# Kernel tuning notes

Measured on AMD Instinct MI355X. Metric: run time of the kernel, lower is better.

## Reference

```python
import jax, jax.numpy as jnp
import numpy as np

B, S, D = 2, 2048, 1024
H = 16            # attention heads
KVH = 4           # key/value heads
G = H // KVH      # group_size = 4
HD = D // H       # head_dim = 64
ROPE_THETA = 10000.0


def rope(x):
    # x: [B, S, D]; interleaved-pair rotary embedding over full last dim
    d = x.shape[-1]
    inv_freq = 1.0 / (ROPE_THETA ** (jnp.arange(0, d, 2, dtype=jnp.float32) / d))  # [d/2]
    ang = jnp.arange(x.shape[1], dtype=jnp.float32)[:, None] * inv_freq[None, :]   # [S, d/2]
    cos, sin = jnp.cos(ang), jnp.sin(ang)
    x1, x2 = x[..., 0::2], x[..., 1::2]
    r1 = x1 * cos - x2 * sin
    r2 = x1 * sin + x2 * cos
    out = jnp.stack([r1, r2], axis=-1).reshape(x.shape)
    return out


def setup_inputs() -> dict:
    key = jax.random.key(0)
    kx, kq, kk, kv = jax.random.split(key, 4)
    x = jax.random.normal(kx, (B, S, D), dtype=jnp.float32)
    # mark last 256 positions of batch element 1 as padding via NaN
    x = x.at[1, S - 256:, :].set(jnp.nan)
    scale = 1.0 / np.sqrt(D)
    Wq = jax.random.normal(kq, (D, D), dtype=jnp.float32) * scale
    Wk = jax.random.normal(kk, (D, D // G), dtype=jnp.float32) * scale
    Wv = jax.random.normal(kv, (D, D // G), dtype=jnp.float32) * scale
    return {"x": x, "Wq": Wq, "Wk": Wk, "Wv": Wv}


def reference(x, Wq, Wk, Wv):
    pad = jnp.isnan(x)                      # [B,S,D]
    x = jnp.where(pad, 0.0, x)
    key_pad = jnp.any(pad, axis=-1)         # [B,S] True = padded token

    q = x @ Wq                              # [B,S,D]
    k = jnp.repeat(x @ Wk, G, axis=-1)      # grouped KV, repeat_interleave -> [B,S,D]
    v = jnp.repeat(x @ Wv, G, axis=-1)

    q = rope(q)
    k = rope(k)

    def split_heads(t):
        return t.reshape(B, S, H, HD).transpose(0, 2, 1, 3)  # [B,H,S,HD]

    q, k, v = split_heads(q), split_heads(k), split_heads(v)

    scores = jnp.einsum('bhqd,bhkd->bhqk', q, k) / np.sqrt(HD)
    causal = jnp.tril(jnp.ones((S, S), dtype=bool))
    allow = causal[None, None, :, :] & (~key_pad)[:, None, None, :]
    scores = jnp.where(allow, scores, -1e9)
    attn = jax.nn.softmax(scores, axis=-1)
    out = jnp.einsum('bhqk,bhkd->bhqd', attn, v)
    return out.transpose(0, 2, 1, 3).reshape(B, S, D)
```

## Files before the change

kernel.cpp:

```cpp
#include <hip/hip_runtime.h>
#include <hip/hip_bf16.h>
#include <math.h>

typedef unsigned short u16;
typedef unsigned int u32;
typedef __bf16 bf16x8 __attribute__((ext_vector_type(8)));
typedef float fx4 __attribute__((ext_vector_type(4)));

#define MFMA16(a, b, c) __builtin_amdgcn_mfma_f32_16x16x32_bf16(a, b, c, 0, 0, 0)

static constexpr int Bb = 2, Ss = 2048, Dd = 1024, Hh = 16, DKV = 256;
static constexpr int NQKV = 1536;
static constexpr int ROWS = Bb * Ss;
static constexpr float L2T_OVER = 0.0259525632f;
static constexpr float SC2 = 0.18033688f;
static constexpr int PSTR = 76;

__device__ __forceinline__ u16 f2bf(float f) {
    union { float f; u32 i; } v; v.f = f;
    u32 u = v.i;
    return (u16)((u + 0x7FFFu + ((u >> 16) & 1u)) >> 16);
}
__device__ __forceinline__ u16 bfr(float f) {
    return (u16)((__float_as_uint(f) + 0x8000u) >> 16);
}

__device__ __forceinline__ void gl16(const u16* g, u16* l) {
    __builtin_amdgcn_global_load_lds(
        (const __attribute__((address_space(1))) void*)g,
        (__attribute__((address_space(3))) void*)l, 16, 0, 0);
}

template <int CTRL>
__device__ __forceinline__ float dppf(float x) {
    return __int_as_float(
        __builtin_amdgcn_mov_dpp(__float_as_int(x), CTRL, 0xF, 0xF, true));
}
__device__ __forceinline__ float rsum16(float x) {
    x += dppf<0xB1>(x);
    x += dppf<0x4E>(x);
    x += dppf<0x124>(x);
    x += dppf<0x128>(x);
    return x;
}

__global__ void pre_kernel(const float* __restrict__ x, const float* __restrict__ Wq,
                           const float* __restrict__ Wk, const float* __restrict__ Wv,
                           u16* __restrict__ xc, u32* __restrict__ kpb,
                           u16* __restrict__ wAll) {
    __shared__ u16 tile[32][33];
    __shared__ int flag;
    int bid = blockIdx.x, t = threadIdx.x;
    if (bid < 4096) {
        int row = bid;
        if (t == 0) flag = 0;
        __syncthreads();
        float4 d = *(const float4*)(x + (size_t)row * Dd + t * 4);
        int any = 0;
        float a0 = d.x, a1 = d.y, a2 = d.z, a3 = d.w;
        if ((__float_as_uint(a0) & 0x7FFFFFFFu) > 0x7F800000u) { a0 = 0.f; any = 1; }
        if ((__float_as_uint(a1) & 0x7FFFFFFFu) > 0x7F800000u) { a1 = 0.f; any = 1; }
        if ((__float_as_uint(a2) & 0x7FFFFFFFu) > 0x7F800000u) { a2 = 0.f; any = 1; }
        if ((__float_as_uint(a3) & 0x7FFFFFFFu) > 0x7F800000u) { a3 = 0.f; any = 1; }
        if (any) atomicOr(&flag, 1);
        uint2 o;
        o.x = (u32)f2bf(a0) | ((u32)f2bf(a1) << 16);
        o.y = (u32)f2bf(a2) | ((u32)f2bf(a3) << 16);
        *(uint2*)(xc + (size_t)row * Dd + t * 4) = o;
        __syncthreads();
        if (t == 0 && flag) {
            int b = row >> 11, s = row & (Ss - 1);
            atomicOr(&kpb[b * 64 + (s >> 5)], 1u << (s & 31));
        }
        return;
    }
    const float* in; u16* out; int C, bx, by;
    if (bid < 5120) { int i = bid - 4096; in = Wq; out = wAll; C = Dd; bx = i & 31; by = i >> 5; }
    else if (bid < 5376) { int i = bid - 5120; in = Wk; out = wAll + (size_t)Dd * Dd; C = DKV; bx = i & 7; by = i >> 3; }
    else { int i = bid - 5376; in = Wv; out = wAll + (size_t)1280 * Dd; C = DKV; bx = i & 7; by = i >> 3; }
    int c0 = bx * 32, r0 = by * 32;
    int tx = t & 31, ty = t >> 5;
    for (int i = 0; i < 32; i += 8)
        tile[ty + i][tx] = f2bf(in[(size_t)(r0 + ty + i) * C + c0 + tx]);
    __syncthreads();
    for (int i = 0; i < 32; i += 8)
        out[(size_t)(c0 + ty + i) * Dd + r0 + tx] = tile[tx][ty + i];
}

__global__ __launch_bounds__(256) void gemm_qkv(
    const u16* __restrict__ A, const u16* __restrict__ Bt, u16* __restrict__ C) {
    __shared__ __align__(16) u16 As[2][128 * 32];
    __shared__ __align__(16) u16 Bs[2][64 * 32];
    int t = threadIdx.x, w = t >> 6, lane = t & 63;
    int l15 = lane & 15, quad = lane >> 4;
    int col0 = blockIdx.x * 64, row0 = blockIdx.y * 128;
    int wm = w >> 1, wn = w & 1;
    fx4 acc[4][2];
#pragma unroll
    for (int i = 0; i < 4; ++i)
#pragma unroll
        for (int j = 0; j < 2; ++j) acc[i][j] = (fx4){0.f, 0.f, 0.f, 0.f};

    auto stage = [&](int kb, int buf) {
#pragma unroll
        for (int i = 0; i < 2; ++i) {
            int slot = i * 256 + t;
            int row = slot >> 2, p = slot & 3, g = p ^ ((row >> 1) & 3);
            gl16(A + (size_t)(row0 + row) * Dd + kb * 32 + g * 8,
                 &As[buf][(i * 256 + w * 64) * 8]);
        }
        {
            int row = t >> 2, p = t & 3, g = p ^ ((row >> 1) & 3);
            gl16(Bt + (size_t)(col0 + row) * Dd + kb * 32 + g * 8,
                 &Bs[buf][(w * 64) * 8]);
        }
    };

    stage(0, 0);
    int buf = 0;
    for (int kb = 0; kb < 32; ++kb) {
        __syncthreads();
        if (kb + 1 < 32) stage(kb + 1, buf ^ 1);
        bf16x8 af[4], bfr2[2];
#pragma unroll
        for (int mi = 0; mi < 4; ++mi) {
            int row = wm * 64 + mi * 16 + l15;
            af[mi] = *(const bf16x8*)(&As[buf][row * 32 + ((quad ^ ((row >> 1) & 3)) * 8)]);
        }
#pragma unroll
        for (int ni = 0; ni < 2; ++ni) {
            int row = wn * 32 + ni * 16 + l15;
            bfr2[ni] = *(const bf16x8*)(&Bs[buf][row * 32 + ((quad ^ ((row >> 1) & 3)) * 8)]);
        }
#pragma unroll
        for (int mi = 0; mi < 4; ++mi)
#pragma unroll
            for (int ni = 0; ni < 2; ++ni)
                acc[mi][ni] = MFMA16(af[mi], bfr2[ni], acc[mi][ni]);
        buf ^= 1;
    }
#pragma unroll
    for (int mi = 0; mi < 4; ++mi) {
        int rbase = row0 + wm * 64 + mi * 16 + quad * 4;
#pragma unroll
        for (int ni = 0; ni < 2; ++ni) {
            int ccol = col0 + wn * 32 + ni * 16 + l15;
#pragma unroll
            for (int r = 0; r < 4; ++r)
                C[(size_t)(rbase + r) * NQKV + ccol] = f2bf(acc[mi][ni][r]);
        }
    }
}

__global__ void post_kernel(const u16* __restrict__ qkv, u16* __restrict__ kr,
                            u16* __restrict__ vtb) {
    __shared__ u16 tile[32][33];
    int bid = blockIdx.x, t = threadIdx.x;
    if (bid < 4096) {
        int row = bid;
        float pos = (float)(row & (Ss - 1));
        float kv = __uint_as_float(((u32)qkv[(size_t)row * NQKV + Dd + t]) << 16);
        float j0 = (float)(2 * t), j1 = j0 + 1.0f;
        float f0 = exp2f(-j0 * L2T_OVER), f1 = exp2f(-j1 * L2T_OVER);
        float s0, c0, s1, c1;
        sincosf(pos * f0, &s0, &c0);
        sincosf(pos * f1, &s1, &c1);
        float r0 = kv * (c0 - s0), r1 = kv * (s0 + c0);
        float r2 = kv * (c1 - s1), r3 = kv * (s1 + c1);
        uint2 o;
        o.x = (u32)f2bf(r0) | ((u32)f2bf(r1) << 16);
        o.y = (u32)f2bf(r2) | ((u32)f2bf(r3) << 16);
        *(uint2*)(kr + (size_t)row * Dd + t * 4) = o;
        return;
    }
    int i = bid - 4096;
    int b = i >> 9, by = (i & 511) >> 3, bx = i & 7;
    int c0 = bx * 32, r0 = by * 32;
    int tx = t & 31, ty = t >> 5;
    for (int k = 0; k < 32; k += 8)
        tile[ty + k][tx] = qkv[(size_t)(b * Ss + r0 + ty + k) * NQKV + 1280 + c0 + tx];
    __syncthreads();
    for (int k = 0; k < 32; k += 8)
        vtb[(size_t)(b * DKV + c0 + ty + k) * Ss + r0 + tx] = tile[tx][ty + k];
}

__device__ __forceinline__ bf16x8 ropeFrag(uint4 raw, float pos, float jbase) {
    u32 W[4] = {raw.x, raw.y, raw.z, raw.w};
    union { u32 u[4]; bf16x8 v; } o;
#pragma unroll
    for (int c = 0; c < 4; ++c) {
        float x0 = __uint_as_float(W[c] << 16);
        float x1 = __uint_as_float(W[c] & 0xFFFF0000u);
        float f = exp2f(-(jbase + (float)c) * L2T_OVER);
        float sn, cs;
        sincosf(pos * f, &sn, &cs);
        float r0 = x0 * cs - x1 * sn, r1 = x0 * sn + x1 * cs;
        o.u[c] = (u32)f2bf(r0) | ((u32)f2bf(r1) << 16);
    }
    return o.v;
}

__global__ __launch_bounds__(256) void attn_kernel(
    const u16* __restrict__ qkv, const u16* __restrict__ kr,
    const u16* __restrict__ vt, const u32* __restrict__ kpb,
    float* __restrict__ out) {
    __shared__ __align__(16) u16 Ks[2][64 * 64];
    __shared__ __align__(16) u16 Vs[2][16 * 64];
    __shared__ __align__(16) u16 Ps[4][16 * PSTR];

    int t = threadIdx.x, w = t >> 6, lane = t & 63;
    int l15 = lane & 15, quad = lane >> 4;
    int bid = blockIdx.x;
    int u = bid >> 5, g = u >> 3, i = u & 7;
    int tile = (g == 0) ? (31 - i) : (g == 1) ? (16 + i) : (g == 2) ? (15 - i) : i;
    int hh = bid & 31, b = hh >> 4, h = hh & 15;
    int q0 = tile * 64;
    int nkb = tile + 1;

    int pos = q0 + w * 16 + l15;
    const u16* qp = qkv + (size_t)(b * Ss + pos) * NQKV + h * 64;
    float jb = (float)(h * 32 + quad * 4);
    bf16x8 qf0 = ropeFrag(*(const uint4*)(qp + quad * 8), (float)pos, jb);
    bf16x8 qf1 = ropeFrag(*(const uint4*)(qp + 32 + quad * 8), (float)pos, jb + 16.f);

    u32 pw_all = kpb[b * 64 + lane];

    auto stageK = [&](int k0, int buf) {
#pragma unroll
        for (int i2 = 0; i2 < 2; ++i2) {
            int row = i2 * 32 + w * 8 + (lane >> 3);
            int gg = (lane & 7) ^ (row & 7);
            gl16(kr + (size_t)(b * Ss + k0 + row) * Dd + h * 64 + gg * 8,
                 &Ks[buf][(i2 * 32 + w * 8) * 64]);
        }
    };
    auto stageV = [&](int k0, int buf) {
        if (w < 2) {
            int row = w * 8 + (lane >> 3);
            int gg = (lane & 7) ^ (row & 7);
            gl16(vt + (size_t)(b * DKV + h * 16 + row) * Ss + k0 + gg * 8,
                 &Vs[buf][(w * 8) * 64]);
        }
    };

    float l_lane[4] = {0.f, 0.f, 0.f, 0.f};
    fx4 oacc = (fx4){0.f, 0.f, 0.f, 0.f};

    stageK(0, 0);
    stageV(0, 0);
    int buf = 0;
    const int qrb = q0 + w * 16 + quad * 4;
    const int qmin = q0 + w * 16;

    for (int kb = 0; kb < nkb; ++kb) {
        int k0 = kb * 64;
        __syncthreads();
        if (kb + 1 < nkb) { stageK(k0 + 64, buf ^ 1); stageV(k0 + 64, buf ^ 1); }

        fx4 s[4];
#pragma unroll
        for (int tt = 0; tt < 4; ++tt) {
            const u16* kb_ = &Ks[buf][(tt * 16 + l15) * 64];
            bf16x8 kf0 = *(const bf16x8*)(kb_ + ((quad ^ (l15 & 7)) * 8));
            bf16x8 kf1 = *(const bf16x8*)(kb_ + (((quad + 4) ^ (l15 & 7)) * 8));
            fx4 z = (fx4){0.f, 0.f, 0.f, 0.f};
            fx4 a = MFMA16(qf0, kf0, z);
            s[tt] = MFMA16(qf1, kf1, a);
        }

        u32 pw0 = (u32)__shfl((int)pw_all, 2 * kb, 64);
        u32 pw1 = (u32)__shfl((int)pw_all, 2 * kb + 1, 64);
        bool fast = (k0 + 63 <= qmin) & ((pw0 | pw1) == 0u);

        float e[4][4];
        if (fast) {
#pragma unroll
            for (int tt = 0; tt < 4; ++tt)
#pragma unroll
                for (int r = 0; r < 4; ++r)
                    e[tt][r] = exp2f(fmaf(s[tt][r], SC2, -32.f));
        } else {
            u32 padb[4];
#pragma unroll
            for (int tt = 0; tt < 4; ++tt)
                padb[tt] = ((tt & 2 ? pw1 : pw0) >> ((tt * 16 + l15) & 31)) & 1u;
#pragma unroll
            for (int r = 0; r < 4; ++r) {
                int qq = qrb + r;
#pragma unroll
                for (int tt = 0; tt < 4; ++tt) {
                    float ee = exp2f(fmaf(s[tt][r], SC2, -32.f));
                    e[tt][r] = (k0 + tt * 16 + l15 <= qq && !padb[tt]) ? ee : 0.f;
                }
            }
        }

#pragma unroll
        for (int r = 0; r < 4; ++r) {
            l_lane[r] += (e[0][r] + e[1][r]) + (e[2][r] + e[3][r]);
            int prow = (quad * 4 + r) * PSTR + l15;
            Ps[w][prow + 0] = bfr(e[0][r]);
            Ps[w][prow + 16] = bfr(e[1][r]);
            Ps[w][prow + 32] = bfr(e[2][r]);
            Ps[w][prow + 48] = bfr(e[3][r]);
        }

#pragma unroll
        for (int hh2 = 0; hh2 < 2; ++hh2) {
            bf16x8 vf = *(const bf16x8*)(&Vs[buf][l15 * 64 + (((quad + 4 * hh2) ^ (l15 & 7)) * 8)]);
            bf16x8 pf = *(const bf16x8*)(&Ps[w][l15 * PSTR + hh2 * 32 + quad * 8]);
            oacc = MFMA16(pf, vf, oacc);
        }
        buf ^= 1;
    }

#pragma unroll
    for (int r = 0; r < 4; ++r) {
        float l_row = rsum16(l_lane[r]);
        float a = oacc[r] / l_row;
        float4 o4 = {a, a, a, a};
        *(float4*)(out + (size_t)(b * Ss + qrb + r) * Dd + h * 64 + l15 * 4) = o4;
    }
}

extern "C" void kernel_launch(void* const* d_in, const int* in_sizes, int n_in,
                              void* d_out, int out_size, void* d_ws, size_t ws_size,
                              hipStream_t stream) {
    const float* x = (const float*)d_in[0];
    const float* Wq = (const float*)d_in[1];
    const float* Wk = (const float*)d_in[2];
    const float* Wv = (const float*)d_in[3];
    float* out = (float*)d_out;

    char* ws = (char*)d_ws;
    const size_t SZ_XC = (size_t)ROWS * Dd * 2;
    const size_t SZ_KPB = 4096;
    const size_t SZ_WALL = (size_t)NQKV * Dd * 2;
    const size_t SZ_QKV = (size_t)ROWS * NQKV * 2;

    size_t off = 0;
    u16* xc = (u16*)(ws + off);
    u16* krope = (u16*)(ws + off); off += SZ_XC;
    u32* kpb = (u32*)(ws + off); off += SZ_KPB;
    u16* wAll = (u16*)(ws + off);
    u16* vtb = (u16*)(ws + off); off += SZ_WALL;
    u16* qkv = (u16*)(ws + off); off += SZ_QKV;
    (void)ws_size; (void)in_sizes; (void)n_in; (void)out_size;

    hipMemsetAsync(kpb, 0, 2 * 64 * 4, stream);
    pre_kernel<<<5632, 256, 0, stream>>>(x, Wq, Wk, Wv, xc, kpb, wAll);
    gemm_qkv<<<dim3(NQKV / 64, ROWS / 128), 256, 0, stream>>>(xc, wAll, qkv);
    post_kernel<<<5120, 256, 0, stream>>>(qkv, krope, vtb);
    attn_kernel<<<1024, 256, 0, stream>>>(qkv, krope, vtb, kpb, out);
}
```

Measured before the change: 152.9 us.

## Pair causal query tiles per block to share K/V staging and balance work

Each attention block now handles two query tiles, p and 31-p. Every block therefore walks the same total number of key blocks, and the K/V tiles it stages in LDS are reused for both query tiles. The grid is halved from 1024 to 512 blocks and the P scratch buffer is doubled. This removes the causal load imbalance and redundant K/V loads for the short tiles. The cost is fewer blocks in flight on a 256-CU part and more registers per thread.

```diff
diff --git a/kernel.cpp b/kernel.cpp
--- a/kernel.cpp
+++ b/kernel.cpp
@@ -206,22 +206,27 @@
     float* __restrict__ out) {
     __shared__ __align__(16) u16 Ks[2][64 * 64];
     __shared__ __align__(16) u16 Vs[2][16 * 64];
-    __shared__ __align__(16) u16 Ps[4][16 * PSTR];
+    __shared__ __align__(16) u16 Ps[4][32 * PSTR];
 
     int t = threadIdx.x, w = t >> 6, lane = t & 63;
     int l15 = lane & 15, quad = lane >> 4;
     int bid = blockIdx.x;
-    int u = bid >> 5, g = u >> 3, i = u & 7;
-    int tile = (g == 0) ? (31 - i) : (g == 1) ? (16 + i) : (g == 2) ? (15 - i) : i;
-    int hh = bid & 31, b = hh >> 4, h = hh & 15;
-    int q0 = tile * 64;
-    int nkb = tile + 1;
-
-    int pos = q0 + w * 16 + l15;
-    const u16* qp = qkv + (size_t)(b * Ss + pos) * NQKV + h * 64;
+    int u = bid >> 4 >> 1;
+    int p = (u < 8) ? (2 * u) : (2 * (u - 8) + 1);
+    int col = bid & 31, b = col >> 4, h = col & 15;
+    int tB = p;
+    int q0A = (31 - p) * 64, q0B = p * 64;
+    int nkb = 32 - p;
+
+    int posA = q0A + w * 16 + l15;
+    int posB = q0B + w * 16 + l15;
+    const u16* qpA = qkv + (size_t)(b * Ss + posA) * NQKV + h * 64;
+    const u16* qpB = qkv + (size_t)(b * Ss + posB) * NQKV + h * 64;
     float jb = (float)(h * 32 + quad * 4);
-    bf16x8 qf0 = ropeFrag(*(const uint4*)(qp + quad * 8), (float)pos, jb);
-    bf16x8 qf1 = ropeFrag(*(const uint4*)(qp + 32 + quad * 8), (float)pos, jb + 16.f);
+    bf16x8 qfA0 = ropeFrag(*(const uint4*)(qpA + quad * 8), (float)posA, jb);
+    bf16x8 qfA1 = ropeFrag(*(const uint4*)(qpA + 32 + quad * 8), (float)posA, jb + 16.f);
+    bf16x8 qfB0 = ropeFrag(*(const uint4*)(qpB + quad * 8), (float)posB, jb);
+    bf16x8 qfB1 = ropeFrag(*(const uint4*)(qpB + 32 + quad * 8), (float)posB, jb + 16.f);
 
     u32 pw_all = kpb[b * 64 + lane];
 
@@ -243,83 +248,137 @@
         }
     };
 
-    float l_lane[4] = {0.f, 0.f, 0.f, 0.f};
-    fx4 oacc = (fx4){0.f, 0.f, 0.f, 0.f};
+    float lA[4] = {0.f, 0.f, 0.f, 0.f}, lB[4] = {0.f, 0.f, 0.f, 0.f};
+    fx4 oA = (fx4){0.f, 0.f, 0.f, 0.f}, oB = (fx4){0.f, 0.f, 0.f, 0.f};
 
     stageK(0, 0);
     stageV(0, 0);
     int buf = 0;
-    const int qrb = q0 + w * 16 + quad * 4;
-    const int qmin = q0 + w * 16;
+    const int qrbA = q0A + w * 16 + quad * 4;
+    const int qrbB = q0B + w * 16 + quad * 4;
+    const int qminA = q0A + w * 16;
+    const int qminB = q0B + w * 16;
 
     for (int kb = 0; kb < nkb; ++kb) {
         int k0 = kb * 64;
         __syncthreads();
         if (kb + 1 < nkb) { stageK(k0 + 64, buf ^ 1); stageV(k0 + 64, buf ^ 1); }
 
-        fx4 s[4];
+        bf16x8 kf0[4], kf1[4];
 #pragma unroll
         for (int tt = 0; tt < 4; ++tt) {
             const u16* kb_ = &Ks[buf][(tt * 16 + l15) * 64];
-            bf16x8 kf0 = *(const bf16x8*)(kb_ + ((quad ^ (l15 & 7)) * 8));
-            bf16x8 kf1 = *(const bf16x8*)(kb_ + (((quad + 4) ^ (l15 & 7)) * 8));
-            fx4 z = (fx4){0.f, 0.f, 0.f, 0.f};
-            fx4 a = MFMA16(qf0, kf0, z);
-            s[tt] = MFMA16(qf1, kf1, a);
-        }
-
+            kf0[tt] = *(const bf16x8*)(kb_ + ((quad ^ (l15 & 7)) * 8));
+            kf1[tt] = *(const bf16x8*)(kb_ + (((quad + 4) ^ (l15 & 7)) * 8));
+        }
         u32 pw0 = (u32)__shfl((int)pw_all, 2 * kb, 64);
         u32 pw1 = (u32)__shfl((int)pw_all, 2 * kb + 1, 64);
-        bool fast = (k0 + 63 <= qmin) & ((pw0 | pw1) == 0u);
-
-        float e[4][4];
-        if (fast) {
-#pragma unroll
-            for (int tt = 0; tt < 4; ++tt)
-#pragma unroll
-                for (int r = 0; r < 4; ++r)
-                    e[tt][r] = exp2f(fmaf(s[tt][r], SC2, -32.f));
-        } else {
-            u32 padb[4];
-#pragma unroll
-            for (int tt = 0; tt < 4; ++tt)
-                padb[tt] = ((tt & 2 ? pw1 : pw0) >> ((tt * 16 + l15) & 31)) & 1u;
+        bool nopad = (pw0 | pw1) == 0u;
+        u32 padb[4];
+#pragma unroll
+        for (int tt = 0; tt < 4; ++tt)
+            padb[tt] = ((tt & 2 ? pw1 : pw0) >> ((tt * 16 + l15) & 31)) & 1u;
+
+        {
+            fx4 s[4];
+#pragma unroll
+            for (int tt = 0; tt < 4; ++tt) {
+                fx4 z = (fx4){0.f, 0.f, 0.f, 0.f};
+                fx4 a = MFMA16(qfA0, kf0[tt], z);
+                s[tt] = MFMA16(qfA1, kf1[tt], a);
+            }
+            bool fast = (k0 + 63 <= qminA) & nopad;
+            float e[4][4];
+            if (fast) {
+#pragma unroll
+                for (int tt = 0; tt < 4; ++tt)
+#pragma unroll
+                    for (int r = 0; r < 4; ++r)
+                        e[tt][r] = exp2f(fmaf(s[tt][r], SC2, -32.f));
+            } else {
+#pragma unroll
+                for (int r = 0; r < 4; ++r) {
+                    int qq = qrbA + r;
+#pragma unroll
+                    for (int tt = 0; tt < 4; ++tt) {
+                        float ee = exp2f(fmaf(s[tt][r], SC2, -32.f));
+                        e[tt][r] = (k0 + tt * 16 + l15 <= qq && !padb[tt]) ? ee : 0.f;
+                    }
+                }
+            }
 #pragma unroll
             for (int r = 0; r < 4; ++r) {
-                int qq = qrb + r;
-#pragma unroll
-                for (int tt = 0; tt < 4; ++tt) {
-                    float ee = exp2f(fmaf(s[tt][r], SC2, -32.f));
-                    e[tt][r] = (k0 + tt * 16 + l15 <= qq && !padb[tt]) ? ee : 0.f;
+                lA[r] += (e[0][r] + e[1][r]) + (e[2][r] + e[3][r]);
+                int prow = (quad * 4 + r) * PSTR + l15;
+                Ps[w][prow + 0] = bfr(e[0][r]);
+                Ps[w][prow + 16] = bfr(e[1][r]);
+                Ps[w][prow + 32] = bfr(e[2][r]);
+                Ps[w][prow + 48] = bfr(e[3][r]);
+            }
+#pragma unroll
+            for (int hh2 = 0; hh2 < 2; ++hh2) {
+                bf16x8 vf = *(const bf16x8*)(&Vs[buf][l15 * 64 + (((quad + 4 * hh2) ^ (l15 & 7)) * 8)]);
+                bf16x8 pf = *(const bf16x8*)(&Ps[w][l15 * PSTR + hh2 * 32 + quad * 8]);
+                oA = MFMA16(pf, vf, oA);
+            }
+        }
+
+        if (kb <= tB) {
+            fx4 s[4];
+#pragma unroll
+            for (int tt = 0; tt < 4; ++tt) {
+                fx4 z = (fx4){0.f, 0.f, 0.f, 0.f};
+                fx4 a = MFMA16(qfB0, kf0[tt], z);
+                s[tt] = MFMA16(qfB1, kf1[tt], a);
+            }
+            bool fast = (k0 + 63 <= qminB) & nopad;
+            float e[4][4];
+            if (fast) {
+#pragma unroll
+                for (int tt = 0; tt < 4; ++tt)
+#pragma unroll
+                    for (int r = 0; r < 4; ++r)
+                        e[tt][r] = exp2f(fmaf(s[tt][r], SC2, -32.f));
+            } else {
+#pragma unroll
+                for (int r = 0; r < 4; ++r) {
+                    int qq = qrbB + r;
+#pragma unroll
+                    for (int tt = 0; tt < 4; ++tt) {
+                        float ee = exp2f(fmaf(s[tt][r], SC2, -32.f));
+                        e[tt][r] = (k0 + tt * 16 + l15 <= qq && !padb[tt]) ? ee : 0.f;
+                    }
                 }
             }
-        }
-
-#pragma unroll
-        for (int r = 0; r < 4; ++r) {
-            l_lane[r] += (e[0][r] + e[1][r]) + (e[2][r] + e[3][r]);
-            int prow = (quad * 4 + r) * PSTR + l15;
-            Ps[w][prow + 0] = bfr(e[0][r]);
-            Ps[w][prow + 16] = bfr(e[1][r]);
-            Ps[w][prow + 32] = bfr(e[2][r]);
-            Ps[w][prow + 48] = bfr(e[3][r]);
-        }
-
-#pragma unroll
-        for (int hh2 = 0; hh2 < 2; ++hh2) {
-            bf16x8 vf = *(const bf16x8*)(&Vs[buf][l15 * 64 + (((quad + 4 * hh2) ^ (l15 & 7)) * 8)]);
-            bf16x8 pf = *(const bf16x8*)(&Ps[w][l15 * PSTR + hh2 * 32 + quad * 8]);
-            oacc = MFMA16(pf, vf, oacc);
+#pragma unroll
+            for (int r = 0; r < 4; ++r) {
+                lB[r] += (e[0][r] + e[1][r]) + (e[2][r] + e[3][r]);
+                int prow = (16 + quad * 4 + r) * PSTR + l15;
+                Ps[w][prow + 0] = bfr(e[0][r]);
+                Ps[w][prow + 16] = bfr(e[1][r]);
+                Ps[w][prow + 32] = bfr(e[2][r]);
+                Ps[w][prow + 48] = bfr(e[3][r]);
+            }
+#pragma unroll
+            for (int hh2 = 0; hh2 < 2; ++hh2) {
+                bf16x8 vf = *(const bf16x8*)(&Vs[buf][l15 * 64 + (((quad + 4 * hh2) ^ (l15 & 7)) * 8)]);
+                bf16x8 pf = *(const bf16x8*)(&Ps[w][(16 + l15) * PSTR + hh2 * 32 + quad * 8]);
+                oB = MFMA16(pf, vf, oB);
+            }
         }
         buf ^= 1;
     }
 
 #pragma unroll
     for (int r = 0; r < 4; ++r) {
-        float l_row = rsum16(l_lane[r]);
-        float a = oacc[r] / l_row;
+        float lrA = rsum16(lA[r]);
+        float a = oA[r] / lrA;
         float4 o4 = {a, a, a, a};
-        *(float4*)(out + (size_t)(b * Ss + qrb + r) * Dd + h * 64 + l15 * 4) = o4;
+        *(float4*)(out + (size_t)(b * Ss + qrbA + r) * Dd + h * 64 + l15 * 4) = o4;
+        float lrB = rsum16(lB[r]);
+        float bb2 = oB[r] / lrB;
+        float4 o5 = {bb2, bb2, bb2, bb2};
+        *(float4*)(out + (size_t)(b * Ss + qrbB + r) * Dd + h * 64 + l15 * 4) = o5;
     }
 }
 
@@ -351,5 +410,5 @@
     pre_kernel<<<5632, 256, 0, stream>>>(x, Wq, Wk, Wv, xc, kpb, wAll);
     gemm_qkv<<<dim3(NQKV / 64, ROWS / 128), 256, 0, stream>>>(xc, wAll, qkv);
     post_kernel<<<5120, 256, 0, stream>>>(qkv, krope, vtb);
-    attn_kernel<<<1024, 256, 0, stream>>>(qkv, krope, vtb, kpb, out);
-}
+    attn_kernel<<<512, 256, 0, stream>>>(qkv, krope, vtb, kpb, out);
+}
```

Result: slower. 156.5 us (+2.4%).
